# Optimization experiments

Hardware: AMD Instinct MI355X
Metric: run time of the kernel (lower is better)

The kernel has to match this reference:

```python
import jax, jax.numpy as jnp
import numpy as np

B, S, HID = 4, 1024, 1024
NH = 16
DH = HID // NH  # 64


def _split_heads(t):
    # [B, S, HID] -> [B, NH, S, DH]
    return t.reshape(B, S, NH, DH).transpose(0, 2, 1, 3)


def _merge_heads(t):
    # [B, NH, S, DH] -> [B, S, HID]
    return t.transpose(0, 2, 1, 3).reshape(B, S, HID)


def setup_inputs() -> dict:
    key = jax.random.key(0)
    ks = jax.random.split(key, 13)
    scale = 1.0 / np.sqrt(HID)
    inp = {"x": jax.random.normal(ks[0], (B, S, HID), dtype=jnp.float32)}
    names = ["Wq", "Wk", "Wv", "Wq2", "Wk2", "Wv2"]
    for i, n in enumerate(names):
        inp[n] = jax.random.normal(ks[1 + i], (HID, HID), dtype=jnp.float32) * scale
        inp["b" + n[1:]] = jax.random.normal(ks[7 + i], (HID,), dtype=jnp.float32) * 0.01
    return inp


def _attn(q, k, v):
    # q,k,v: [B, NH, S, DH]
    scores = jnp.einsum("bhqd,bhkd->bhqk", q, k) / np.sqrt(DH).astype(np.float32)
    probs = jax.nn.softmax(scores, axis=-1)
    return jnp.einsum("bhqk,bhkd->bhqd", probs, v)


def reference(x, Wq, bq, Wk, bk, Wv, bv, Wq2, bq2, Wk2, bk2, Wv2, bv2):
    # nn.Linear: y = x @ W.T + b
    q1 = _split_heads(x @ Wq.T + bq)
    k1 = _split_heads(x @ Wk.T + bk)
    v1 = _split_heads(x @ Wv.T + bv)
    q2 = _split_heads(x @ Wq2.T + bq2)
    k2 = _split_heads(x @ Wk2.T + bk2)
    v2 = _split_heads(x @ Wv2.T + bv2)
    # 5'UTR direction: q1 attends to k2/v2; 3'UTR direction: q2 attends to k1/v1
    out5 = _merge_heads(_attn(q1, k2, v2))
    out3 = _merge_heads(_attn(q2, k1, v1))
    return (out5, out3)
```

## Files before the change

### kernel.cpp

```cpp
#include <hip/hip_runtime.h>


typedef __attribute__((ext_vector_type(8))) short bf16x8;
typedef __attribute__((ext_vector_type(4))) short bf16x4;
typedef __attribute__((ext_vector_type(4))) float f32x4;
typedef __attribute__((ext_vector_type(4))) short s16x4;

#define MFMA16(a, b, c) __builtin_amdgcn_mfma_f32_16x16x32_bf16(a, b, c, 0, 0, 0)

__device__ __forceinline__ f32x4 mfma16k(bf16x4 a, bf16x4 b, f32x4 c) {
#if __has_builtin(__builtin_amdgcn_mfma_f32_16x16x16bf16_1k)
  return __builtin_amdgcn_mfma_f32_16x16x16bf16_1k(a, b, c, 0, 0, 0);
#elif __has_builtin(__builtin_amdgcn_mfma_f32_16x16x16_bf16)
  return __builtin_amdgcn_mfma_f32_16x16x16_bf16(a, b, c, 0, 0, 0);
#else
  asm volatile("v_mfma_f32_16x16x16_bf16 %0, %1, %2, %0"
               : "+v"(c) : "v"(a), "v"(b));
  return c;
#endif
}

__device__ __forceinline__ unsigned short f2bf(float f) {
  unsigned u = __float_as_uint(f);
  u = (u + 0x7fffu + ((u >> 16) & 1u)) >> 16;
  return (unsigned short)u;
}

__device__ __forceinline__ unsigned cvt_pk_bf16(float lo, float hi) {
  unsigned r;
  asm("v_cvt_pk_bf16_f32 %0, %1, %2" : "=v"(r) : "v"(lo), "v"(hi));
  return r;
}

__device__ __forceinline__ void gll16(const void* g, void* l) {
  __builtin_amdgcn_global_load_lds(
      (const __attribute__((address_space(1))) unsigned int*)g,
      (__attribute__((address_space(3))) unsigned int*)l, 16, 0, 0);
}

__global__ __launch_bounds__(256) void convert_k(
    const float* __restrict__ x,
    const float* __restrict__ W0, const float* __restrict__ W1,
    const float* __restrict__ W2, const float* __restrict__ W3,
    const float* __restrict__ W4, const float* __restrict__ W5,
    short* __restrict__ xbf, short* __restrict__ wbf) {
  const int tid = blockIdx.x * 256 + threadIdx.x;
  const int e = tid << 2;
  const float* src;
  short* dst;
  int off;
  if (e < (4 << 20)) {
    src = x; dst = xbf; off = e;
  } else {
    const int j = e - (4 << 20);
    const int wsel = j >> 20;
    off = j & ((1 << 20) - 1);
    src = (wsel == 0) ? W0 : (wsel == 1) ? W1 : (wsel == 2) ? W2
        : (wsel == 3) ? W3 : (wsel == 4) ? W4 : W5;
    dst = wbf + ((size_t)wsel << 20);
  }
  const float4 v = *(const float4*)(src + off);
  s16x4 o;
  o.x = (short)f2bf(v.x);
  o.y = (short)f2bf(v.y);
  o.z = (short)f2bf(v.z);
  o.w = (short)f2bf(v.w);
  *(s16x4*)(dst + off) = o;
}

__global__ __launch_bounds__(256) void proj_gemm(
    const short* __restrict__ A, const short* __restrict__ W,
    const float* __restrict__ bq, const float* __restrict__ bk,
    const float* __restrict__ bv, const float* __restrict__ bq2,
    const float* __restrict__ bk2, const float* __restrict__ bv2,
    short* __restrict__ qkv) {
  __shared__ __align__(16) short As[2][128 * 64];
  __shared__ __align__(16) short Bs[2][128 * 64];
  const int wg = blockIdx.x;
  const int xcd = wg & 7, i = wg >> 3;
  const int mb = i / 6, j = i - mb * 6;
  const int panel = xcd * 6 + j;
  const int p = panel >> 3, n_ = panel & 7;
  const int m0 = mb << 7, n0 = n_ << 7;

  const short* B = W + ((size_t)p << 20);
  const int t = threadIdx.x, lane = t & 63, w = t >> 6;
  const int g = lane >> 4, lr = lane & 15;
  const int srow = (w << 5) + (lane >> 3);
  const int scol = (lane & 7) << 3;
  const int wm = ((w >> 1) << 6), wn = ((w & 1) << 6);
  f32x4 acc[4][4] = {};

  auto stage = [&](int k0, int buf) {
#pragma unroll
    for (int ii = 0; ii < 4; ++ii) {
      gll16(A + (size_t)(m0 + srow + ii * 8) * 1024 + k0 + scol,
            &As[buf][(w << 11) + (ii << 9)]);
      gll16(B + (size_t)(n0 + srow + ii * 8) * 1024 + k0 + scol,
            &Bs[buf][(w << 11) + (ii << 9)]);
    }
  };

  stage(0, 0);
  asm volatile("s_waitcnt vmcnt(0)" ::: "memory");
  __builtin_amdgcn_s_barrier();

  int cur = 0;
  for (int kt = 0; kt < 16; ++kt) {
    if (kt < 15) stage((kt + 1) << 6, cur ^ 1);
#pragma unroll
    for (int kk = 0; kk < 2; ++kk) {
      bf16x8 af[4], bfm[4];
#pragma unroll
      for (int mi = 0; mi < 4; ++mi)
        af[mi] = *(const bf16x8*)
            &As[cur][(wm + mi * 16 + lr) * 64 + kk * 32 + g * 8];
#pragma unroll
      for (int nj = 0; nj < 4; ++nj)
        bfm[nj] = *(const bf16x8*)
            &Bs[cur][(wn + nj * 16 + lr) * 64 + kk * 32 + g * 8];
      __builtin_amdgcn_s_setprio(1);
#pragma unroll
      for (int mi = 0; mi < 4; ++mi)
#pragma unroll
        for (int nj = 0; nj < 4; ++nj)
          acc[mi][nj] = MFMA16(af[mi], bfm[nj], acc[mi][nj]);
      __builtin_amdgcn_s_setprio(0);
    }
    asm volatile("s_waitcnt vmcnt(0)" ::: "memory");
    __builtin_amdgcn_s_barrier();
    cur ^= 1;
  }

  const float* bias = (p == 0) ? bq : (p == 1) ? bk : (p == 2) ? bv
                    : (p == 3) ? bq2 : (p == 4) ? bk2 : bv2;
  const int ptype = (p == 0 || p == 3) ? 0 : (p == 1 || p == 4) ? 1 : 2;
  unsigned short* dst = (unsigned short*)qkv + ((size_t)p << 22);
#pragma unroll
  for (int nj = 0; nj < 4; ++nj) {
    const int n = n0 + wn + nj * 16 + lr;
    const float bb = bias[n];
    const int h = n >> 6, d = n & 63;
#pragma unroll
    for (int mi = 0; mi < 4; ++mi) {
#pragma unroll
      for (int r = 0; r < 4; ++r) {
        const int m = m0 + wm + mi * 16 + (g << 2) + r;
        const int b = m >> 10, s = m & 1023;
        const unsigned short val = f2bf(acc[mi][nj][r] + bb);
        size_t idx;
        if (ptype == 0) {
          idx = ((size_t)(((b << 4) + h) * 1024 + s) << 6) + d;
        } else if (ptype == 1) {
          const int d2 = (d & 7) | (((d >> 3) ^ (s & 7)) << 3);
          idx = ((size_t)(((b << 4) + h) * 1024 + s) << 6) + d2;
        } else {
          const int tt = s >> 6, s2 = s & 63;
          const int s3 = (s2 & 7) | (((s2 >> 3) ^ (d & 7)) << 3);
          idx = ((size_t)((((b << 4) + h) * 16 + tt) * 64 + d) << 6) + s3;
        }
        dst[idx] = val;
      }
    }
  }
}

__global__ __launch_bounds__(256) void attn_k(const short* __restrict__ qkv,
                                              float* __restrict__ out) {
  __shared__ __align__(16) short Ks[2][64 * 64];
  __shared__ __align__(16) short Vs[2][64 * 64];

  const int L = blockIdx.x;
  const int xcd = L & 7, ss = L >> 3;
  const int qt = ss & 15, pg = ss >> 4;
  const int pp = xcd + (pg << 3);
  const int hb = pp & 63, dir = pp >> 6;

  const short* Q = qkv + ((size_t)(dir ? 3 : 0) << 22) + ((size_t)hb << 16);
  const short* K = qkv + ((size_t)(dir ? 1 : 4) << 22) + ((size_t)hb << 16);
  const short* V = qkv + ((size_t)(dir ? 2 : 5) << 22) + ((size_t)hb << 16);
  float* O = out + ((size_t)dir << 22);

  const int t = threadIdx.x, lane = t & 63, w = t >> 6;
  const int g = lane >> 4, lr = lane & 15;

  const int qrow = (qt << 6) + (w << 4) + lr;
  bf16x8 qf[2];
  qf[0] = *(const bf16x8*)(Q + qrow * 64 + g * 8);
  qf[1] = *(const bf16x8*)(Q + qrow * 64 + 32 + g * 8);

  const bf16x4 ones4 = {0x3F80, 0x3F80, 0x3F80, 0x3F80};

  f32x4 oacc[4] = {};
  f32x4 lacc = {};
  float mrun = -3.0e38f;
  const float CSC = 0.18033688f;

  const int srow = (w << 4) + (lane >> 3);
  const int scol = (lane & 7) << 3;

  auto stage = [&](int kt, int buf) {
#pragma unroll
    for (int i = 0; i < 2; ++i) {
      gll16(K + (size_t)((kt << 6) + srow + i * 8) * 64 + scol,
            &Ks[buf][(w << 10) + (i << 9)]);
      gll16(V + (size_t)(kt << 12) + (size_t)(srow + i * 8) * 64 + scol,
            &Vs[buf][(w << 10) + (i << 9)]);
    }
  };

  stage(0, 0);
  asm volatile("s_waitcnt vmcnt(0)" ::: "memory");
  __builtin_amdgcn_s_barrier();

  int cur = 0;
  for (int kt = 0; kt < 16; ++kt) {
    if (kt < 15) stage(kt + 1, cur ^ 1);

    f32x4 sc2[4] = {};
    __builtin_amdgcn_s_setprio(1);
#pragma unroll
    for (int dk = 0; dk < 2; ++dk) {
#pragma unroll
      for (int kn = 0; kn < 4; ++kn) {
        const int krow = kn * 16 + lr;
        const bf16x8 kf = *(const bf16x8*)
            &Ks[cur][krow * 64 +
                     ((((dk << 6) + (g << 4)) ^ ((krow & 7) << 4)) >> 1)];
        sc2[kn] = MFMA16(kf, qf[dk], sc2[kn]);
      }
    }
    __builtin_amdgcn_s_setprio(0);

    float tm = fmaxf(fmaxf(fmaxf(sc2[0][0], sc2[0][1]),
                           fmaxf(sc2[0][2], sc2[0][3])),
                     fmaxf(fmaxf(sc2[1][0], sc2[1][1]),
                           fmaxf(sc2[1][2], sc2[1][3])));
    tm = fmaxf(tm, fmaxf(fmaxf(fmaxf(sc2[2][0], sc2[2][1]),
                               fmaxf(sc2[2][2], sc2[2][3])),
                         fmaxf(fmaxf(sc2[3][0], sc2[3][1]),
                               fmaxf(sc2[3][2], sc2[3][3]))));
    const bool ok = __all(fmaf(tm, CSC, -mrun) <= 8.0f);
    if (!ok) {
      float t2 = fmaxf(tm, __shfl_xor(tm, 16));
      t2 = fmaxf(t2, __shfl_xor(t2, 32));
      const float mnew = fmaxf(mrun, t2 * CSC);
      const float scq = exp2f(mrun - mnew);
      mrun = mnew;
#pragma unroll
      for (int r = 0; r < 4; ++r) {
        const float sr = __shfl(scq, (g << 2) + r);
        lacc[r] *= sr;
#pragma unroll
        for (int dn = 0; dn < 4; ++dn) oacc[dn][r] *= sr;
      }
    }

    bf16x4 pa[4];
#pragma unroll
    for (int kn = 0; kn < 4; ++kn) {
      const float p0 = exp2f(fmaf(sc2[kn][0], CSC, -mrun));
      const float p1 = exp2f(fmaf(sc2[kn][1], CSC, -mrun));
      const float p2 = exp2f(fmaf(sc2[kn][2], CSC, -mrun));
      const float p3 = exp2f(fmaf(sc2[kn][3], CSC, -mrun));
      union { unsigned u[2]; bf16x4 v; } pk;
      pk.u[0] = cvt_pk_bf16(p0, p1);
      pk.u[1] = cvt_pk_bf16(p2, p3);
      pa[kn] = pk.v;
    }

    __builtin_amdgcn_s_setprio(1);
#pragma unroll
    for (int kn = 0; kn < 4; ++kn) {
      lacc = mfma16k(pa[kn], ones4, lacc);
#pragma unroll
      for (int dn = 0; dn < 4; ++dn) {
        const int vrow = dn * 16 + lr;
        const int ch = (2 * kn + (g >> 1)) ^ (vrow & 7);
        const bf16x4 vf = *(const bf16x4*)
            &Vs[cur][vrow * 64 + ch * 8 + ((g & 1) << 2)];
        oacc[dn] = mfma16k(pa[kn], vf, oacc[dn]);
      }
    }
    __builtin_amdgcn_s_setprio(0);

    asm volatile("s_waitcnt vmcnt(0)" ::: "memory");
    __builtin_amdgcn_s_barrier();
    cur ^= 1;
  }

  const int b = hb >> 4, h = hb & 15;
  float rl[4];
#pragma unroll
  for (int r = 0; r < 4; ++r) rl[r] = 1.0f / lacc[r];
#pragma unroll
  for (int dn = 0; dn < 4; ++dn) {
#pragma unroll
    for (int r = 0; r < 4; ++r) {
      const int q = (qt << 6) + (w << 4) + (g << 2) + r;
      const int d = dn * 16 + lr;
      O[((size_t)(b * 1024 + q) << 10) + h * 64 + d] = oacc[dn][r] * rl[r];
    }
  }
}

extern "C" void kernel_launch(void* const* d_in, const int* in_sizes, int n_in,
                              void* d_out, int out_size, void* d_ws,
                              size_t ws_size, hipStream_t stream) {
  const float* x   = (const float*)d_in[0];
  const float* Wq  = (const float*)d_in[1];
  const float* bq  = (const float*)d_in[2];
  const float* Wk  = (const float*)d_in[3];
  const float* bk  = (const float*)d_in[4];
  const float* Wv  = (const float*)d_in[5];
  const float* bv  = (const float*)d_in[6];
  const float* Wq2 = (const float*)d_in[7];
  const float* bq2 = (const float*)d_in[8];
  const float* Wk2 = (const float*)d_in[9];
  const float* bk2 = (const float*)d_in[10];
  const float* Wv2 = (const float*)d_in[11];
  const float* bv2 = (const float*)d_in[12];

  char* ws = (char*)d_ws;
  short* xbf = (short*)ws;
  short* wbf = (short*)(ws + 8388608);
  short* qkv = (short*)(ws + 20971520);

  convert_k<<<10240, 256, 0, stream>>>(x, Wq, Wk, Wv, Wq2, Wk2, Wv2, xbf, wbf);
  proj_gemm<<<1536, 256, 0, stream>>>(xbf, wbf, bq, bk, bv, bq2, bk2,
                                      bv2, qkv);
  attn_k<<<2048, 256, 0, stream>>>(qkv, (float*)d_out);
}
```

Measured before the change: 174.5 us.

## Rewrite projection GEMM as 256x256 tile, 8-wave kernel with swizzled LDS

Replaces the 128x128, 4-wave projection GEMM with a 256x256-tile, 512-thread kernel. Each wave computes four 128x128 quadrant sub-tiles in phases, and global-to-LDS loads for the next k-step are interleaved between those MFMA phases under fine-grained vmcnt waits and barriers. LDS rows are XOR-swizzled to avoid bank conflicts. The larger tile cuts global traffic per FLOP and should improve overlap, but the grid drops to 384 blocks, which may leave some CUs idle, and the extra barriers add synchronisation cost.

```diff
diff --git a/kernel.cpp b/kernel.cpp
--- a/kernel.cpp
+++ b/kernel.cpp
@@ -68,68 +68,133 @@
   *(s16x4*)(dst + off) = o;
 }
 
-__global__ __launch_bounds__(256) void proj_gemm(
-    const short* __restrict__ A, const short* __restrict__ W,
+#define STAGE_A(T, H)                                                     \
+  {                                                                       \
+    const int k0s = (T) << 6;                                             \
+    _Pragma("unroll") for (int ii = 0; ii < 2; ++ii) {                    \
+      const int slot = ((H) << 10) + (w << 7) + (ii << 6) + lane;         \
+      const int rr = slot >> 3;                                           \
+      const int gc = (slot & 7) ^ (rr & 7);                               \
+      gll16(Ag + (size_t)(m0 + rr) * 1024 + k0s + (gc << 3),              \
+            &As[(T) & 1][((H) << 13) + (w << 10) + (ii << 9)]);           \
+    }                                                                     \
+  }
+
+#define STAGE_B(T, H)                                                     \
+  {                                                                       \
+    const int k0s = (T) << 6;                                             \
+    _Pragma("unroll") for (int ii = 0; ii < 2; ++ii) {                    \
+      const int slot = ((H) << 10) + (w << 7) + (ii << 6) + lane;         \
+      const int rr = slot >> 3;                                           \
+      const int gc = (slot & 7) ^ (rr & 7);                               \
+      gll16(Bg + (size_t)(nbase + rr) * 1024 + k0s + (gc << 3),           \
+            &Bs[(T) & 1][((H) << 13) + (w << 10) + (ii << 9)]);           \
+    }                                                                     \
+  }
+
+#define DS_LOADS(MH, NH, TB)                                              \
+  bf16x8 af[4][2], bfr[2][2];                                             \
+  _Pragma("unroll") for (int mi = 0; mi < 4; ++mi)                        \
+    _Pragma("unroll") for (int kk = 0; kk < 2; ++kk) {                    \
+      const int rA = (MH) * 128 + wr * 64 + mi * 16 + lr;                 \
+      af[mi][kk] = *(const bf16x8*)                                       \
+          &As[TB][rA * 64 + ((((kk << 2) + g) ^ (rA & 7)) << 3)];         \
+    }                                                                     \
+  _Pragma("unroll") for (int ni = 0; ni < 2; ++ni)                        \
+    _Pragma("unroll") for (int kk = 0; kk < 2; ++kk) {                    \
+      const int rB = (NH) * 128 + wc * 32 + ni * 16 + lr;                 \
+      bfr[ni][kk] = *(const bf16x8*)                                      \
+          &Bs[TB][rB * 64 + ((((kk << 2) + g) ^ (rB & 7)) << 3)];         \
+    }
+
+#define MFMA_PHASE(MH, NH)                                                \
+  __builtin_amdgcn_s_barrier();                                           \
+  __builtin_amdgcn_s_setprio(1);                                          \
+  _Pragma("unroll") for (int mi = 0; mi < 4; ++mi)                        \
+    _Pragma("unroll") for (int ni = 0; ni < 2; ++ni)                      \
+      _Pragma("unroll") for (int kk = 0; kk < 2; ++kk)                    \
+        acc[MH][NH][mi][ni] =                                             \
+            MFMA16(af[mi][kk], bfr[ni][kk], acc[MH][NH][mi][ni]);         \
+  __builtin_amdgcn_s_setprio(0);                                          \
+  __builtin_amdgcn_s_barrier();
+
+__global__ __launch_bounds__(512, 2) void proj_gemm8(
+    const short* __restrict__ Ag, const short* __restrict__ W,
     const float* __restrict__ bq, const float* __restrict__ bk,
     const float* __restrict__ bv, const float* __restrict__ bq2,
     const float* __restrict__ bk2, const float* __restrict__ bv2,
     short* __restrict__ qkv) {
-  __shared__ __align__(16) short As[2][128 * 64];
-  __shared__ __align__(16) short Bs[2][128 * 64];
-  const int wg = blockIdx.x;
-  const int xcd = wg & 7, i = wg >> 3;
-  const int mb = i / 6, j = i - mb * 6;
-  const int panel = xcd * 6 + j;
-  const int p = panel >> 3, n_ = panel & 7;
-  const int m0 = mb << 7, n0 = n_ << 7;
-
-  const short* B = W + ((size_t)p << 20);
+  __shared__ __align__(16) short As[2][16384];
+  __shared__ __align__(16) short Bs[2][16384];
+
+  const int bid = blockIdx.x;
+  const int xcd = bid & 7, i = bid >> 3;
+  const int nb = xcd * 3 + (i >> 4);
+  const int mbv = i & 15;
+  const int m0 = mbv << 8;
+  const int p = nb >> 2;
+  const int nbase = (nb & 3) << 8;
+
+  const short* Bg = W + ((size_t)p << 20);
   const int t = threadIdx.x, lane = t & 63, w = t >> 6;
   const int g = lane >> 4, lr = lane & 15;
-  const int srow = (w << 5) + (lane >> 3);
-  const int scol = (lane & 7) << 3;
-  const int wm = ((w >> 1) << 6), wn = ((w & 1) << 6);
-  f32x4 acc[4][4] = {};
-
-  auto stage = [&](int k0, int buf) {
-#pragma unroll
-    for (int ii = 0; ii < 4; ++ii) {
-      gll16(A + (size_t)(m0 + srow + ii * 8) * 1024 + k0 + scol,
-            &As[buf][(w << 11) + (ii << 9)]);
-      gll16(B + (size_t)(n0 + srow + ii * 8) * 1024 + k0 + scol,
-            &Bs[buf][(w << 11) + (ii << 9)]);
-    }
-  };
-
-  stage(0, 0);
-  asm volatile("s_waitcnt vmcnt(0)" ::: "memory");
+  const int wr = w >> 2, wc = w & 3;
+
+  f32x4 acc[2][2][4][2] = {};
+
+  STAGE_A(0, 0); STAGE_B(0, 0); STAGE_A(0, 1); STAGE_B(0, 1);
+  STAGE_A(1, 0); STAGE_B(1, 0);
+  asm volatile("s_waitcnt vmcnt(4)" ::: "memory");
   __builtin_amdgcn_s_barrier();
 
-  int cur = 0;
-  for (int kt = 0; kt < 16; ++kt) {
-    if (kt < 15) stage((kt + 1) << 6, cur ^ 1);
-#pragma unroll
-    for (int kk = 0; kk < 2; ++kk) {
-      bf16x8 af[4], bfm[4];
-#pragma unroll
-      for (int mi = 0; mi < 4; ++mi)
-        af[mi] = *(const bf16x8*)
-            &As[cur][(wm + mi * 16 + lr) * 64 + kk * 32 + g * 8];
-#pragma unroll
-      for (int nj = 0; nj < 4; ++nj)
-        bfm[nj] = *(const bf16x8*)
-            &Bs[cur][(wn + nj * 16 + lr) * 64 + kk * 32 + g * 8];
-      __builtin_amdgcn_s_setprio(1);
-#pragma unroll
-      for (int mi = 0; mi < 4; ++mi)
-#pragma unroll
-        for (int nj = 0; nj < 4; ++nj)
-          acc[mi][nj] = MFMA16(af[mi], bfm[nj], acc[mi][nj]);
-      __builtin_amdgcn_s_setprio(0);
-    }
-    asm volatile("s_waitcnt vmcnt(0)" ::: "memory");
-    __builtin_amdgcn_s_barrier();
-    cur ^= 1;
+  for (int j = 0; j < 8; ++j) {
+    const bool u = j < 7;
+    {
+      DS_LOADS(0, 0, 0);
+      STAGE_A(2 * j + 1, 1); STAGE_B(2 * j + 1, 1);
+      MFMA_PHASE(0, 0);
+    }
+    {
+      DS_LOADS(0, 1, 0);
+      MFMA_PHASE(0, 1);
+    }
+    {
+      DS_LOADS(1, 0, 0);
+      if (u) STAGE_A(2 * j + 2, 0);
+      MFMA_PHASE(1, 0);
+    }
+    {
+      DS_LOADS(1, 1, 0);
+      if (u) {
+        STAGE_B(2 * j + 2, 0);
+        asm volatile("s_waitcnt vmcnt(4)" ::: "memory");
+      } else {
+        asm volatile("s_waitcnt vmcnt(0)" ::: "memory");
+      }
+      MFMA_PHASE(1, 1);
+    }
+    {
+      DS_LOADS(0, 0, 1);
+      if (u) { STAGE_A(2 * j + 2, 1); STAGE_B(2 * j + 2, 1); }
+      MFMA_PHASE(0, 0);
+    }
+    {
+      DS_LOADS(0, 1, 1);
+      MFMA_PHASE(0, 1);
+    }
+    {
+      DS_LOADS(1, 0, 1);
+      if (u) STAGE_A(2 * j + 3, 0);
+      MFMA_PHASE(1, 0);
+    }
+    {
+      DS_LOADS(1, 1, 1);
+      if (u) {
+        STAGE_B(2 * j + 3, 0);
+        asm volatile("s_waitcnt vmcnt(4)" ::: "memory");
+      }
+      MFMA_PHASE(1, 1);
+    }
   }
 
   const float* bias = (p == 0) ? bq : (p == 1) ? bk : (p == 2) ? bv
@@ -137,29 +202,35 @@
   const int ptype = (p == 0 || p == 3) ? 0 : (p == 1 || p == 4) ? 1 : 2;
   unsigned short* dst = (unsigned short*)qkv + ((size_t)p << 22);
 #pragma unroll
-  for (int nj = 0; nj < 4; ++nj) {
-    const int n = n0 + wn + nj * 16 + lr;
-    const float bb = bias[n];
-    const int h = n >> 6, d = n & 63;
-#pragma unroll
-    for (int mi = 0; mi < 4; ++mi) {
-#pragma unroll
-      for (int r = 0; r < 4; ++r) {
-        const int m = m0 + wm + mi * 16 + (g << 2) + r;
-        const int b = m >> 10, s = m & 1023;
-        const unsigned short val = f2bf(acc[mi][nj][r] + bb);
-        size_t idx;
-        if (ptype == 0) {
-          idx = ((size_t)(((b << 4) + h) * 1024 + s) << 6) + d;
-        } else if (ptype == 1) {
-          const int d2 = (d & 7) | (((d >> 3) ^ (s & 7)) << 3);
-          idx = ((size_t)(((b << 4) + h) * 1024 + s) << 6) + d2;
-        } else {
-          const int tt = s >> 6, s2 = s & 63;
-          const int s3 = (s2 & 7) | (((s2 >> 3) ^ (d & 7)) << 3);
-          idx = ((size_t)((((b << 4) + h) * 16 + tt) * 64 + d) << 6) + s3;
+  for (int nh = 0; nh < 2; ++nh) {
+#pragma unroll
+    for (int ni = 0; ni < 2; ++ni) {
+      const int nn = nbase + nh * 128 + wc * 32 + ni * 16 + lr;
+      const float bb = bias[nn];
+      const int h = nn >> 6, d = nn & 63;
+#pragma unroll
+      for (int mh = 0; mh < 2; ++mh) {
+#pragma unroll
+        for (int mi = 0; mi < 4; ++mi) {
+#pragma unroll
+          for (int r = 0; r < 4; ++r) {
+            const int m = m0 + mh * 128 + wr * 64 + mi * 16 + (g << 2) + r;
+            const int b = m >> 10, s = m & 1023;
+            const unsigned short val = f2bf(acc[mh][nh][mi][ni][r] + bb);
+            size_t idx;
+            if (ptype == 0) {
+              idx = ((size_t)(((b << 4) + h) * 1024 + s) << 6) + d;
+            } else if (ptype == 1) {
+              const int d2 = (d & 7) | (((d >> 3) ^ (s & 7)) << 3);
+              idx = ((size_t)(((b << 4) + h) * 1024 + s) << 6) + d2;
+            } else {
+              const int tt = s >> 6, s2 = s & 63;
+              const int s3 = (s2 & 7) | (((s2 >> 3) ^ (d & 7)) << 3);
+              idx = ((size_t)((((b << 4) + h) * 16 + tt) * 64 + d) << 6) + s3;
+            }
+            dst[idx] = val;
+          }
         }
-        dst[idx] = val;
       }
     }
   }
@@ -327,7 +398,7 @@
   short* qkv = (short*)(ws + 20971520);
 
   convert_k<<<10240, 256, 0, stream>>>(x, Wq, Wk, Wv, Wq2, Wk2, Wv2, xbf, wbf);
-  proj_gemm<<<1536, 256, 0, stream>>>(xbf, wbf, bq, bk, bv, bq2, bk2,
+  proj_gemm8<<<384, 512, 0, stream>>>(xbf, wbf, bq, bk, bv, bq2, bk2,
                                       bv2, qkv);
   attn_k<<<2048, 256, 0, stream>>>(qkv, (float*)d_out);
 }
```

Result: slower. 204.5 us (+17.2%).

## Triple-buffer projection GEMM with BK=32 tiles and XOR-swizzled LDS

Applied to the files above, without the earlier changes.

Reworks the projection GEMM's main loop to use K-tiles of 32 in a three-stage LDS ring buffer, keeping two tiles of global loads in flight with a partial vmcnt wait. Staging uses an XOR swizzle on 16-byte chunks to reduce LDS bank conflicts on fragment reads. It also changes the block-to-tile mapping so consecutive blocks on an XCD share an N panel, and requests 3 waves per SIMD via launch bounds. The cost is twice as many barriers per K, and possible register pressure from the occupancy hint.

```diff
diff --git a/kernel.cpp b/kernel.cpp
--- a/kernel.cpp
+++ b/kernel.cpp
@@ -68,68 +68,79 @@
   *(s16x4*)(dst + off) = o;
 }
 
-__global__ __launch_bounds__(256) void proj_gemm(
-    const short* __restrict__ A, const short* __restrict__ W,
+__global__ __launch_bounds__(256, 3) void proj_gemm32(
+    const short* __restrict__ Ag, const short* __restrict__ W,
     const float* __restrict__ bq, const float* __restrict__ bk,
     const float* __restrict__ bv, const float* __restrict__ bq2,
     const float* __restrict__ bk2, const float* __restrict__ bv2,
     short* __restrict__ qkv) {
-  __shared__ __align__(16) short As[2][128 * 64];
-  __shared__ __align__(16) short Bs[2][128 * 64];
-  const int wg = blockIdx.x;
-  const int xcd = wg & 7, i = wg >> 3;
-  const int mb = i / 6, j = i - mb * 6;
-  const int panel = xcd * 6 + j;
-  const int p = panel >> 3, n_ = panel & 7;
-  const int m0 = mb << 7, n0 = n_ << 7;
-
-  const short* B = W + ((size_t)p << 20);
+  __shared__ __align__(16) short As[3][128 * 32];
+  __shared__ __align__(16) short Bs[3][128 * 32];
+
+  const int bid = blockIdx.x;
+  const int xcd = bid & 7, i = bid >> 3;
+  const int nb = xcd * 6 + (i >> 5);
+  const int mb = i & 31;
+  const int p = nb >> 3;
+  const int n0 = (nb & 7) << 7, m0 = mb << 7;
+
+  const short* Bg = W + ((size_t)p << 20);
   const int t = threadIdx.x, lane = t & 63, w = t >> 6;
   const int g = lane >> 4, lr = lane & 15;
-  const int srow = (w << 5) + (lane >> 3);
-  const int scol = (lane & 7) << 3;
   const int wm = ((w >> 1) << 6), wn = ((w & 1) << 6);
+
   f32x4 acc[4][4] = {};
 
-  auto stage = [&](int k0, int buf) {
-#pragma unroll
-    for (int ii = 0; ii < 4; ++ii) {
-      gll16(A + (size_t)(m0 + srow + ii * 8) * 1024 + k0 + scol,
-            &As[buf][(w << 11) + (ii << 9)]);
-      gll16(B + (size_t)(n0 + srow + ii * 8) * 1024 + k0 + scol,
-            &Bs[buf][(w << 11) + (ii << 9)]);
+  auto stage = [&](int kt, int buf) {
+    const int k0 = kt << 5;
+#pragma unroll
+    for (int ld = 0; ld < 2; ++ld) {
+      const int slot = ld * 256 + t;
+      const int rr = slot >> 2;
+      const int gc = (slot & 3) ^ (rr & 3);
+      gll16(Ag + (size_t)(m0 + rr) * 1024 + k0 + (gc << 3),
+            &As[buf][slot * 8]);
+      gll16(Bg + (size_t)(n0 + rr) * 1024 + k0 + (gc << 3),
+            &Bs[buf][slot * 8]);
     }
   };
 
   stage(0, 0);
-  asm volatile("s_waitcnt vmcnt(0)" ::: "memory");
+  stage(1, 1);
+  asm volatile("s_waitcnt vmcnt(4)" ::: "memory");
   __builtin_amdgcn_s_barrier();
 
-  int cur = 0;
-  for (int kt = 0; kt < 16; ++kt) {
-    if (kt < 15) stage((kt + 1) << 6, cur ^ 1);
-#pragma unroll
-    for (int kk = 0; kk < 2; ++kk) {
-      bf16x8 af[4], bfm[4];
-#pragma unroll
-      for (int mi = 0; mi < 4; ++mi)
-        af[mi] = *(const bf16x8*)
-            &As[cur][(wm + mi * 16 + lr) * 64 + kk * 32 + g * 8];
+  int buf = 0;
+  for (int T = 0; T < 32; ++T) {
+    if (T <= 29) stage(T + 2, (T + 2) % 3);
+
+    bf16x8 af[4], bfr[4];
+#pragma unroll
+    for (int mi = 0; mi < 4; ++mi) {
+      const int rA = wm + mi * 16 + lr;
+      af[mi] = *(const bf16x8*)&As[buf][rA * 32 + ((g ^ (rA & 3)) << 3)];
+    }
+#pragma unroll
+    for (int nj = 0; nj < 4; ++nj) {
+      const int rB = wn + nj * 16 + lr;
+      bfr[nj] = *(const bf16x8*)&Bs[buf][rB * 32 + ((g ^ (rB & 3)) << 3)];
+    }
+
+    __builtin_amdgcn_s_setprio(1);
+#pragma unroll
+    for (int mi = 0; mi < 4; ++mi)
 #pragma unroll
       for (int nj = 0; nj < 4; ++nj)
-        bfm[nj] = *(const bf16x8*)
-            &Bs[cur][(wn + nj * 16 + lr) * 64 + kk * 32 + g * 8];
-      __builtin_amdgcn_s_setprio(1);
-#pragma unroll
-      for (int mi = 0; mi < 4; ++mi)
-#pragma unroll
-        for (int nj = 0; nj < 4; ++nj)
-          acc[mi][nj] = MFMA16(af[mi], bfm[nj], acc[mi][nj]);
-      __builtin_amdgcn_s_setprio(0);
-    }
-    asm volatile("s_waitcnt vmcnt(0)" ::: "memory");
+        acc[mi][nj] = MFMA16(af[mi], bfr[nj], acc[mi][nj]);
+    __builtin_amdgcn_s_setprio(0);
+
+    if (T <= 29) {
+      asm volatile("s_waitcnt vmcnt(4)" ::: "memory");
+    } else if (T == 30) {
+      asm volatile("s_waitcnt vmcnt(0)" ::: "memory");
+    }
     __builtin_amdgcn_s_barrier();
-    cur ^= 1;
+    buf = (buf == 2) ? 0 : buf + 1;
   }
 
   const float* bias = (p == 0) ? bq : (p == 1) ? bk : (p == 2) ? bv
@@ -327,7 +338,7 @@
   short* qkv = (short*)(ws + 20971520);
 
   convert_k<<<10240, 256, 0, stream>>>(x, Wq, Wk, Wv, Wq2, Wk2, Wv2, xbf, wbf);
-  proj_gemm<<<1536, 256, 0, stream>>>(xbf, wbf, bq, bk, bv, bq2, bk2,
-                                      bv2, qkv);
+  proj_gemm32<<<1536, 256, 0, stream>>>(xbf, wbf, bq, bk, bv, bq2, bk2,
+                                        bv2, qkv);
   attn_k<<<2048, 256, 0, stream>>>(qkv, (float*)d_out);
 }
```

After: 170.1 us. 2.5% less time.
